# Performance work log

Measured on AMD Instinct MI355X. Metric: run time of the kernel, lower is better.

## Reference

```python
import jax, jax.numpy as jnp
import numpy as np

B, H, W, C_IN, C_HID = 32, 64, 64, 384, 128

def setup_inputs() -> dict:
    key = jax.random.key(0)
    k0, k1, k2 = jax.random.split(key, 3)
    dino_features = jax.random.normal(k0, (B, H, W, C_IN), dtype=jnp.float32)
    # Xavier-uniform(gain=0.5) bounds for conv weights, HWIO layout
    fan1 = C_IN * 9 + C_HID * 9
    lim1 = 0.5 * np.sqrt(6.0 / fan1)
    W1 = jax.random.uniform(k1, (3, 3, C_IN, C_HID), minval=-lim1, maxval=lim1, dtype=jnp.float32)
    b1 = jnp.zeros((C_HID,), dtype=jnp.float32)
    fan2 = C_HID + 1
    lim2 = 0.5 * np.sqrt(6.0 / fan2)
    W2 = jax.random.uniform(k2, (1, 1, C_HID, 1), minval=-lim2, maxval=lim2, dtype=jnp.float32)
    b2 = jnp.zeros((1,), dtype=jnp.float32)
    return {"dino_features": dino_features, "W1": W1, "b1": b1, "W2": W2, "b2": b2}

def _conv(x, w, pad):
    # x: NHWC, w: HWIO -> NHWC
    return jax.lax.conv_general_dilated(
        x, w, window_strides=(1, 1), padding=pad,
        dimension_numbers=("NHWC", "HWIO", "NHWC"))

def reference(dino_features, W1, b1, W2, b2):
    # conv3x3 (pad 1) -> ReLU -> conv1x1 -> sigmoid; output (B,H,W,1)
    h = jax.nn.relu(_conv(dino_features, W1, ((1, 1), (1, 1))) + b1)
    logits = _conv(h, W2, ((0, 0), (0, 0))) + b2
    return jax.nn.sigmoid(logits)
```

## Files before the change

kernel.cpp:

```cpp
#include <hip/hip_runtime.h>
#include <hip/hip_bf16.h>
#include <math.h>


typedef __attribute__((ext_vector_type(8))) unsigned short ushort8;
typedef __attribute__((ext_vector_type(8))) __bf16 bf16x8;
typedef __attribute__((ext_vector_type(4))) float floatx4;

#define HPX 324
#define BUFE 10368

static __device__ __forceinline__ unsigned short f2bf_rne(float f) {
  union { float f; unsigned int u; } x; x.f = f;
  unsigned int u = x.u;
  return (unsigned short)((u + 0x7fffu + ((u >> 16) & 1u)) >> 16);
}

static __device__ __forceinline__ ushort8 pack8(const float* v) {
  ushort8 r;
#pragma unroll
  for (int i = 0; i < 4; ++i) {
    __hip_bfloat162 p = __float22bfloat162_rn(make_float2(v[2 * i], v[2 * i + 1]));
    union { __hip_bfloat162 b; unsigned int u; } c;
    c.b = p;
    r[2 * i] = (unsigned short)(c.u & 0xffffu);
    r[2 * i + 1] = (unsigned short)(c.u >> 16);
  }
  return r;
}

__global__ void prep_w1_kernel(const float* __restrict__ W1,
                               unsigned short* __restrict__ W1b) {
  __shared__ unsigned short tile[32 * 128];
  const int kk = blockIdx.x;
  const int o = kk / 12;
  const int chunk = kk - o * 12;
  const float* src = W1 + (o * 384 + chunk * 32) * 128;
  const int t = threadIdx.x;
#pragma unroll
  for (int i = 0; i < 16; ++i) {
    int idx = t + i * 256;
    int c = idx >> 7;
    int n = idx & 127;
    tile[n * 32 + c] = f2bf_rne(src[idx]);
  }
  __syncthreads();
  unsigned short* dst = W1b + kk * 4096;
#pragma unroll
  for (int i = 0; i < 16; ++i) {
    int idx = t + i * 256;
    dst[idx] = tile[idx];
  }
}

__global__ __launch_bounds__(512, 3) void conv_fused_kernel(
    const float* __restrict__ x, const unsigned short* __restrict__ W1b,
    const float* __restrict__ b1, const float* __restrict__ W2,
    const float* __restrict__ b2, float* __restrict__ out) {
  __shared__ alignas(16) unsigned short Ah[2 * BUFE];
  __shared__ float hsum[256 * 4];

  const int t = threadIdx.x;
  const int w = t >> 6;
  const int wm = w >> 2;
  const int wn = w & 3;
  const int lane = t & 63;
  const int g = lane >> 4;
  const int lr = lane & 15;

  const int img = blockIdx.x >> 4;
  const int tileId = blockIdx.x & 15;
  const int ty0 = (tileId >> 2) << 4;
  const int tx0 = (tileId & 3) << 4;

  int smask = 0;
  int soff[3];
#pragma unroll
  for (int j = 0; j < 3; ++j) {
    int item = t + (j << 9);
    int px = item >> 2, sub = item & 3;
    int hy = (px * 57) >> 10;
    int hx = px - hy * 18;
    int iy = ty0 + hy - 1, ix = tx0 + hx - 1;
    int v = (item < 1296) && ((unsigned)iy < 64u) && ((unsigned)ix < 64u);
    smask |= (v << j);
    int iyc = v ? iy : 0, ixc = v ? ix : 0;
    soff[j] = ((((img << 6) + iyc) << 6) + ixc) * 384 + sub * 8;
  }

  const int boff = ((wn * 32 + lr) << 5) + (g << 3);
  const int aoffl = (lr << 5) + (g << 3);

  floatx4 acc[8][2] = {};

  const float b1v0 = b1[wn * 32 + lr];
  const float b1v1 = b1[wn * 32 + 16 + lr];
  const float w2v0 = W2[wn * 32 + lr];
  const float w2v1 = W2[wn * 32 + 16 + lr];

  float sg1[8];
  float sr[2][8];

  {
    if (smask & 1) {
      *(float4*)&sg1[0] = *(const float4*)(x + soff[0]);
      *(float4*)&sg1[4] = *(const float4*)(x + soff[0] + 4);
    } else {
#pragma unroll
      for (int e = 0; e < 8; ++e) sg1[e] = 0.0f;
    }
#pragma unroll
    for (int j = 0; j < 2; ++j) {
      const int jj = 1 + j;
      if ((smask >> jj) & 1) {
        *(float4*)&sr[j][0] = *(const float4*)(x + soff[jj]);
        *(float4*)&sr[j][4] = *(const float4*)(x + soff[jj] + 4);
      } else {
#pragma unroll
        for (int e = 0; e < 8; ++e) sr[j][e] = 0.0f;
      }
    }
    *(ushort8*)&Ah[t << 3] = pack8(sg1);
    *(ushort8*)&Ah[(t + 512) << 3] = pack8(sr[0]);
    if (t < 272) *(ushort8*)&Ah[(t + 1024) << 3] = pack8(sr[1]);
  }
  __syncthreads();

  for (int c = 0; c < 12; ++c) {
    const int rb = (c & 1) * BUFE;
    const int wb = BUFE - rb;
    const int choff = (c + 1) << 5;
    const bool pf = (c < 11);

#pragma unroll
    for (int ox = 0; ox < 3; ++ox) {
      bf16x8 bf[3][2];
#pragma unroll
      for (int oy = 0; oy < 3; ++oy) {
        const unsigned short* bp =
            W1b + (((oy * 3 + ox) * 12 + c) << 12) + boff;
        bf[oy][0] = *(const bf16x8*)bp;
        bf[oy][1] = *(const bf16x8*)(bp + 512);
      }

      if (ox == 0) {
        if (pf) {
          if (smask & 1) {
            *(float4*)&sg1[0] = *(const float4*)(x + soff[0] + choff);
            *(float4*)&sg1[4] = *(const float4*)(x + soff[0] + choff + 4);
          } else {
#pragma unroll
            for (int e = 0; e < 8; ++e) sg1[e] = 0.0f;
          }
        }
      } else if (ox == 1) {
        if (pf) {
          *(ushort8*)&Ah[wb + (t << 3)] = pack8(sg1);
#pragma unroll
          for (int j = 0; j < 2; ++j) {
            const int jj = 1 + j;
            if ((smask >> jj) & 1) {
              *(float4*)&sr[j][0] = *(const float4*)(x + soff[jj] + choff);
              *(float4*)&sr[j][4] = *(const float4*)(x + soff[jj] + choff + 4);
            } else {
#pragma unroll
              for (int e = 0; e < 8; ++e) sr[j][e] = 0.0f;
            }
          }
        }
      } else {
        if (pf) {
          *(ushort8*)&Ah[wb + ((t + 512) << 3)] = pack8(sr[0]);
          if (t < 272) *(ushort8*)&Ah[wb + ((t + 1024) << 3)] = pack8(sr[1]);
        }
      }

      __builtin_amdgcn_s_setprio(1);
#pragma unroll
      for (int hl = 0; hl < 10; ++hl) {
        const int hg = wm * 8 + hl;
        const bf16x8 af =
            *(const bf16x8*)&Ah[rb + ((hg * 18 + ox) << 5) + aoffl];
#pragma unroll
        for (int oy = 0; oy < 3; ++oy) {
          const int mi = hl - oy;
          if (mi >= 0 && mi < 8) {
            acc[mi][0] = __builtin_amdgcn_mfma_f32_16x16x32_bf16(
                af, bf[oy][0], acc[mi][0], 0, 0, 0);
            acc[mi][1] = __builtin_amdgcn_mfma_f32_16x16x32_bf16(
                af, bf[oy][1], acc[mi][1], 0, 0, 0);
          }
        }
      }
      __builtin_amdgcn_s_setprio(0);
    }
    __syncthreads();
  }

#pragma unroll
  for (int mi = 0; mi < 8; ++mi) {
#pragma unroll
    for (int r = 0; r < 4; ++r) {
      float h0 = fmaxf(acc[mi][0][r] + b1v0, 0.0f);
      float h1 = fmaxf(acc[mi][1][r] + b1v1, 0.0f);
      float v = h0 * w2v0 + h1 * w2v1;
      v += __shfl_xor(v, 1);
      v += __shfl_xor(v, 2);
      v += __shfl_xor(v, 4);
      v += __shfl_xor(v, 8);
      if (lr == 0) {
        int m = (wm * 8 + mi) * 16 + g * 4 + r;
        hsum[m * 4 + wn] = v;
      }
    }
  }
  __syncthreads();
  if (t < 256) {
    float4 p = *(const float4*)&hsum[t * 4];
    float s = p.x + p.y + p.z + p.w + b2[0];
    float sig = 1.0f / (1.0f + expf(-s));
    int prow = t >> 4, pcol = t & 15;
    out[((((img << 6) + ty0 + prow) << 6) + tx0 + pcol)] = sig;
  }
}

extern "C" void kernel_launch(void* const* d_in, const int* in_sizes, int n_in,
                              void* d_out, int out_size, void* d_ws, size_t ws_size,
                              hipStream_t stream) {
  const float* x  = (const float*)d_in[0];
  const float* W1 = (const float*)d_in[1];
  const float* b1 = (const float*)d_in[2];
  const float* W2 = (const float*)d_in[3];
  const float* b2 = (const float*)d_in[4];
  float* out = (float*)d_out;
  unsigned short* W1b = (unsigned short*)d_ws;

  prep_w1_kernel<<<108, 256, 0, stream>>>(W1, W1b);
  conv_fused_kernel<<<512, 512, 0, stream>>>(x, W1b, b1, W2, b2, out);
}
```

Baseline: 342.4 us.

## Halve conv tile to 8x16 pixels and software-pipeline weight register prefetch

Shrinks each block from 16x16 to 8x16 output pixels with 256 threads (4 waves across hidden channels, no row split), doubling grid size to 1024 blocks. The channel loop is unrolled by two with explicit double-buffered register prefetch of the W1 fragments one ox-step ahead, interleaved with the global loads and LDS writes of the next input chunk. The goal is to hide global weight-load latency behind MFMAs and improve occupancy and load balance. The trade-off is a larger halo fraction (10x18 for 8x16 vs 18x18 for 16x16), which means more redundant input loads per output pixel, plus higher register pressure from the two weight buffers.

```diff
diff --git a/kernel.cpp b/kernel.cpp
--- a/kernel.cpp
+++ b/kernel.cpp
@@ -7,8 +7,8 @@
 typedef __attribute__((ext_vector_type(8))) __bf16 bf16x8;
 typedef __attribute__((ext_vector_type(4))) float floatx4;
 
-#define HPX 324
-#define BUFE 10368
+#define HPX2 180
+#define E 5760
 
 static __device__ __forceinline__ unsigned short f2bf_rne(float f) {
   union { float f; unsigned int u; } x; x.f = f;
@@ -53,147 +53,139 @@
   }
 }
 
-__global__ __launch_bounds__(512, 3) void conv_fused_kernel(
+#define SLOAD(DST, JJ, CHOFF)                                                \
+  if ((smask >> (JJ)) & 1) {                                                 \
+    *(float4*)&DST[0] = *(const float4*)(x + soff[JJ] + (CHOFF));            \
+    *(float4*)&DST[4] = *(const float4*)(x + soff[JJ] + (CHOFF) + 4);        \
+  } else {                                                                   \
+    _Pragma("unroll") for (int e = 0; e < 8; ++e) DST[e] = 0.0f;             \
+  }
+
+#define SWRITE(SRC, JJ, WB)                                                  \
+  if ((JJ) < 2 || t < 208)                                                   \
+    *(ushort8*)&Ah[(WB) + ((t + ((JJ) << 8)) << 3)] = pack8(SRC);
+
+#define PREFETCH_B(BUF, OX, CC)                                              \
+  _Pragma("unroll") for (int oy = 0; oy < 3; ++oy) {                         \
+    const unsigned short* bp =                                               \
+        W1b + (((oy * 3 + (OX)) * 12 + (CC)) << 12) + boff;                  \
+    BUF[oy * 2 + 0] = *(const bf16x8*)bp;                                    \
+    BUF[oy * 2 + 1] = *(const bf16x8*)(bp + 512);                            \
+  }
+
+#define MFMA_BLOCK(RB, OX, BUF)                                              \
+  __builtin_amdgcn_s_setprio(1);                                             \
+  _Pragma("unroll") for (int hl = 0; hl < 10; ++hl) {                        \
+    const bf16x8 af =                                                        \
+        *(const bf16x8*)&Ah[(RB) + ((hl * 18 + (OX)) << 5) + aoffl];         \
+    _Pragma("unroll") for (int oy = 0; oy < 3; ++oy) {                       \
+      const int mi = hl - oy;                                                \
+      if (mi >= 0 && mi < 8) {                                               \
+        acc[mi][0] = __builtin_amdgcn_mfma_f32_16x16x32_bf16(                \
+            af, BUF[oy * 2 + 0], acc[mi][0], 0, 0, 0);                       \
+        acc[mi][1] = __builtin_amdgcn_mfma_f32_16x16x32_bf16(                \
+            af, BUF[oy * 2 + 1], acc[mi][1], 0, 0, 0);                       \
+      }                                                                      \
+    }                                                                        \
+  }                                                                          \
+  __builtin_amdgcn_s_setprio(0);
+
+__global__ __launch_bounds__(256, 3) void conv_fused_kernel(
     const float* __restrict__ x, const unsigned short* __restrict__ W1b,
     const float* __restrict__ b1, const float* __restrict__ W2,
     const float* __restrict__ b2, float* __restrict__ out) {
-  __shared__ alignas(16) unsigned short Ah[2 * BUFE];
-  __shared__ float hsum[256 * 4];
+  __shared__ alignas(16) unsigned short Ah[2 * E];
+  __shared__ float hsum[128 * 4];
 
   const int t = threadIdx.x;
   const int w = t >> 6;
-  const int wm = w >> 2;
-  const int wn = w & 3;
   const int lane = t & 63;
   const int g = lane >> 4;
   const int lr = lane & 15;
 
-  const int img = blockIdx.x >> 4;
-  const int tileId = blockIdx.x & 15;
-  const int ty0 = (tileId >> 2) << 4;
-  const int tx0 = (tileId & 3) << 4;
+  const int img = blockIdx.x >> 5;
+  const int tid = blockIdx.x & 31;
+  const int ty0 = (tid >> 2) << 3;
+  const int tx0 = (tid & 3) << 4;
 
   int smask = 0;
   int soff[3];
 #pragma unroll
   for (int j = 0; j < 3; ++j) {
-    int item = t + (j << 9);
+    int item = t + (j << 8);
     int px = item >> 2, sub = item & 3;
     int hy = (px * 57) >> 10;
     int hx = px - hy * 18;
     int iy = ty0 + hy - 1, ix = tx0 + hx - 1;
-    int v = (item < 1296) && ((unsigned)iy < 64u) && ((unsigned)ix < 64u);
+    int v = (item < 720) && ((unsigned)iy < 64u) && ((unsigned)ix < 64u);
     smask |= (v << j);
     int iyc = v ? iy : 0, ixc = v ? ix : 0;
     soff[j] = ((((img << 6) + iyc) << 6) + ixc) * 384 + sub * 8;
   }
 
-  const int boff = ((wn * 32 + lr) << 5) + (g << 3);
+  const int boff = ((w * 32 + lr) << 5) + (g << 3);
   const int aoffl = (lr << 5) + (g << 3);
 
   floatx4 acc[8][2] = {};
 
-  const float b1v0 = b1[wn * 32 + lr];
-  const float b1v1 = b1[wn * 32 + 16 + lr];
-  const float w2v0 = W2[wn * 32 + lr];
-  const float w2v1 = W2[wn * 32 + 16 + lr];
-
-  float sg1[8];
-  float sr[2][8];
+  const float b1v0 = b1[w * 32 + lr];
+  const float b1v1 = b1[w * 32 + 16 + lr];
+  const float w2v0 = W2[w * 32 + lr];
+  const float w2v1 = W2[w * 32 + 16 + lr];
+
+  float sA[8], sB[8];
+  bf16x8 bfU[6], bfV[6];
 
   {
-    if (smask & 1) {
-      *(float4*)&sg1[0] = *(const float4*)(x + soff[0]);
-      *(float4*)&sg1[4] = *(const float4*)(x + soff[0] + 4);
-    } else {
-#pragma unroll
-      for (int e = 0; e < 8; ++e) sg1[e] = 0.0f;
+    SLOAD(sA, 0, 0)
+    SLOAD(sB, 1, 0)
+    SWRITE(sA, 0, 0)
+    SLOAD(sA, 2, 0)
+    SWRITE(sB, 1, 0)
+    SWRITE(sA, 2, 0)
+    PREFETCH_B(bfU, 0, 0)
+  }
+  __syncthreads();
+
+  for (int c = 0; c < 12; c += 2) {
+    const int cB = c + 1;
+    const bool pfB = (c < 10);
+    const int chA = (c + 1) << 5;
+    const int chB = (c + 2) << 5;
+
+    PREFETCH_B(bfV, 1, c)
+    SLOAD(sA, 0, chA)
+    MFMA_BLOCK(0, 0, bfU)
+
+    PREFETCH_B(bfU, 2, c)
+    SLOAD(sB, 1, chA)
+    SWRITE(sA, 0, E)
+    MFMA_BLOCK(0, 1, bfV)
+
+    PREFETCH_B(bfV, 0, cB)
+    SLOAD(sA, 2, chA)
+    SWRITE(sB, 1, E)
+    MFMA_BLOCK(0, 2, bfU)
+
+    SWRITE(sA, 2, E)
+    __syncthreads();
+
+    PREFETCH_B(bfU, 1, cB)
+    if (pfB) { SLOAD(sA, 0, chB) }
+    MFMA_BLOCK(E, 0, bfV)
+
+    PREFETCH_B(bfV, 2, cB)
+    if (pfB) { SLOAD(sB, 1, chB) SWRITE(sA, 0, 0) }
+    MFMA_BLOCK(E, 1, bfU)
+
+    {
+      const int cn = (c + 2 < 12) ? c + 2 : 11;
+      PREFETCH_B(bfU, 0, cn)
     }
-#pragma unroll
-    for (int j = 0; j < 2; ++j) {
-      const int jj = 1 + j;
-      if ((smask >> jj) & 1) {
-        *(float4*)&sr[j][0] = *(const float4*)(x + soff[jj]);
-        *(float4*)&sr[j][4] = *(const float4*)(x + soff[jj] + 4);
-      } else {
-#pragma unroll
-        for (int e = 0; e < 8; ++e) sr[j][e] = 0.0f;
-      }
-    }
-    *(ushort8*)&Ah[t << 3] = pack8(sg1);
-    *(ushort8*)&Ah[(t + 512) << 3] = pack8(sr[0]);
-    if (t < 272) *(ushort8*)&Ah[(t + 1024) << 3] = pack8(sr[1]);
-  }
-  __syncthreads();
-
-  for (int c = 0; c < 12; ++c) {
-    const int rb = (c & 1) * BUFE;
-    const int wb = BUFE - rb;
-    const int choff = (c + 1) << 5;
-    const bool pf = (c < 11);
-
-#pragma unroll
-    for (int ox = 0; ox < 3; ++ox) {
-      bf16x8 bf[3][2];
-#pragma unroll
-      for (int oy = 0; oy < 3; ++oy) {
-        const unsigned short* bp =
-            W1b + (((oy * 3 + ox) * 12 + c) << 12) + boff;
-        bf[oy][0] = *(const bf16x8*)bp;
-        bf[oy][1] = *(const bf16x8*)(bp + 512);
-      }
-
-      if (ox == 0) {
-        if (pf) {
-          if (smask & 1) {
-            *(float4*)&sg1[0] = *(const float4*)(x + soff[0] + choff);
-            *(float4*)&sg1[4] = *(const float4*)(x + soff[0] + choff + 4);
-          } else {
-#pragma unroll
-            for (int e = 0; e < 8; ++e) sg1[e] = 0.0f;
-          }
-        }
-      } else if (ox == 1) {
-        if (pf) {
-          *(ushort8*)&Ah[wb + (t << 3)] = pack8(sg1);
-#pragma unroll
-          for (int j = 0; j < 2; ++j) {
-            const int jj = 1 + j;
-            if ((smask >> jj) & 1) {
-              *(float4*)&sr[j][0] = *(const float4*)(x + soff[jj] + choff);
-              *(float4*)&sr[j][4] = *(const float4*)(x + soff[jj] + choff + 4);
-            } else {
-#pragma unroll
-              for (int e = 0; e < 8; ++e) sr[j][e] = 0.0f;
-            }
-          }
-        }
-      } else {
-        if (pf) {
-          *(ushort8*)&Ah[wb + ((t + 512) << 3)] = pack8(sr[0]);
-          if (t < 272) *(ushort8*)&Ah[wb + ((t + 1024) << 3)] = pack8(sr[1]);
-        }
-      }
-
-      __builtin_amdgcn_s_setprio(1);
-#pragma unroll
-      for (int hl = 0; hl < 10; ++hl) {
-        const int hg = wm * 8 + hl;
-        const bf16x8 af =
-            *(const bf16x8*)&Ah[rb + ((hg * 18 + ox) << 5) + aoffl];
-#pragma unroll
-        for (int oy = 0; oy < 3; ++oy) {
-          const int mi = hl - oy;
-          if (mi >= 0 && mi < 8) {
-            acc[mi][0] = __builtin_amdgcn_mfma_f32_16x16x32_bf16(
-                af, bf[oy][0], acc[mi][0], 0, 0, 0);
-            acc[mi][1] = __builtin_amdgcn_mfma_f32_16x16x32_bf16(
-                af, bf[oy][1], acc[mi][1], 0, 0, 0);
-          }
-        }
-      }
-      __builtin_amdgcn_s_setprio(0);
-    }
+    if (pfB) { SLOAD(sA, 2, chB) SWRITE(sB, 1, 0) }
+    MFMA_BLOCK(E, 2, bfV)
+
+    if (pfB) { SWRITE(sA, 2, 0) }
     __syncthreads();
   }
 
@@ -209,13 +201,13 @@
       v += __shfl_xor(v, 4);
       v += __shfl_xor(v, 8);
       if (lr == 0) {
-        int m = (wm * 8 + mi) * 16 + g * 4 + r;
-        hsum[m * 4 + wn] = v;
+        int m = mi * 16 + g * 4 + r;
+        hsum[m * 4 + w] = v;
       }
     }
   }
   __syncthreads();
-  if (t < 256) {
+  if (t < 128) {
     float4 p = *(const float4*)&hsum[t * 4];
     float s = p.x + p.y + p.z + p.w + b2[0];
     float sig = 1.0f / (1.0f + expf(-s));
@@ -236,5 +228,5 @@
   unsigned short* W1b = (unsigned short*)d_ws;
 
   prep_w1_kernel<<<108, 256, 0, stream>>>(W1, W1b);
-  conv_fused_kernel<<<512, 512, 0, stream>>>(x, W1b, b1, W2, b2, out);
-}
+  conv_fused_kernel<<<1024, 256, 0, stream>>>(x, W1b, b1, W2, b2, out);
+}
```

Measured after the change: 335.2 us. 2.1% less time.

## Pack staged input to bf16 in registers and raise occupancy to 4 blocks

Applied to the files above, without the earlier changes.

Staged input values are now converted to packed bf16 right after the global load, so only 4 registers per slot stay live instead of 8 floats. The three staging slots are spread evenly across the ox iterations, with the last write moved after the MFMA loop. The bias and W2 loads move to the epilogue, and launch bounds rise from 3 to 4 blocks per CU to use the lower register pressure. The risk is register spills or less latency hiding for the global loads, since each load now has a shorter window before it is consumed.

```diff
diff --git a/kernel.cpp b/kernel.cpp
--- a/kernel.cpp
+++ b/kernel.cpp
@@ -53,7 +53,23 @@
   }
 }
 
-__global__ __launch_bounds__(512, 3) void conv_fused_kernel(
+#define SLOADP(DST, JJ, CHOFF)                                               \
+  {                                                                          \
+    float tf[8];                                                             \
+    if ((smask >> (JJ)) & 1) {                                               \
+      *(float4*)&tf[0] = *(const float4*)(x + soff[JJ] + (CHOFF));           \
+      *(float4*)&tf[4] = *(const float4*)(x + soff[JJ] + (CHOFF) + 4);       \
+    } else {                                                                 \
+      _Pragma("unroll") for (int e = 0; e < 8; ++e) tf[e] = 0.0f;            \
+    }                                                                        \
+    DST = pack8(tf);                                                         \
+  }
+
+#define SWRITE8(SRC, JJ, WB)                                                 \
+  if ((JJ) < 2 || t < 272)                                                   \
+    *(ushort8*)&Ah[(WB) + ((t + ((JJ) << 9)) << 3)] = SRC;
+
+__global__ __launch_bounds__(512, 4) void conv_fused_kernel(
     const float* __restrict__ x, const unsigned short* __restrict__ W1b,
     const float* __restrict__ b1, const float* __restrict__ W2,
     const float* __restrict__ b2, float* __restrict__ out) {
@@ -93,36 +109,15 @@
 
   floatx4 acc[8][2] = {};
 
-  const float b1v0 = b1[wn * 32 + lr];
-  const float b1v1 = b1[wn * 32 + 16 + lr];
-  const float w2v0 = W2[wn * 32 + lr];
-  const float w2v1 = W2[wn * 32 + 16 + lr];
-
-  float sg1[8];
-  float sr[2][8];
+  ushort8 su0, su1, su2;
 
   {
-    if (smask & 1) {
-      *(float4*)&sg1[0] = *(const float4*)(x + soff[0]);
-      *(float4*)&sg1[4] = *(const float4*)(x + soff[0] + 4);
-    } else {
-#pragma unroll
-      for (int e = 0; e < 8; ++e) sg1[e] = 0.0f;
-    }
-#pragma unroll
-    for (int j = 0; j < 2; ++j) {
-      const int jj = 1 + j;
-      if ((smask >> jj) & 1) {
-        *(float4*)&sr[j][0] = *(const float4*)(x + soff[jj]);
-        *(float4*)&sr[j][4] = *(const float4*)(x + soff[jj] + 4);
-      } else {
-#pragma unroll
-        for (int e = 0; e < 8; ++e) sr[j][e] = 0.0f;
-      }
-    }
-    *(ushort8*)&Ah[t << 3] = pack8(sg1);
-    *(ushort8*)&Ah[(t + 512) << 3] = pack8(sr[0]);
-    if (t < 272) *(ushort8*)&Ah[(t + 1024) << 3] = pack8(sr[1]);
+    SLOADP(su0, 0, 0)
+    SLOADP(su1, 1, 0)
+    SLOADP(su2, 2, 0)
+    SWRITE8(su0, 0, 0)
+    SWRITE8(su1, 1, 0)
+    SWRITE8(su2, 2, 0)
   }
   __syncthreads();
 
@@ -143,35 +138,15 @@
         bf[oy][1] = *(const bf16x8*)(bp + 512);
       }
 
-      if (ox == 0) {
-        if (pf) {
-          if (smask & 1) {
-            *(float4*)&sg1[0] = *(const float4*)(x + soff[0] + choff);
-            *(float4*)&sg1[4] = *(const float4*)(x + soff[0] + choff + 4);
-          } else {
-#pragma unroll
-            for (int e = 0; e < 8; ++e) sg1[e] = 0.0f;
-          }
-        }
-      } else if (ox == 1) {
-        if (pf) {
-          *(ushort8*)&Ah[wb + (t << 3)] = pack8(sg1);
-#pragma unroll
-          for (int j = 0; j < 2; ++j) {
-            const int jj = 1 + j;
-            if ((smask >> jj) & 1) {
-              *(float4*)&sr[j][0] = *(const float4*)(x + soff[jj] + choff);
-              *(float4*)&sr[j][4] = *(const float4*)(x + soff[jj] + choff + 4);
-            } else {
-#pragma unroll
-              for (int e = 0; e < 8; ++e) sr[j][e] = 0.0f;
-            }
-          }
-        }
-      } else {
-        if (pf) {
-          *(ushort8*)&Ah[wb + ((t + 512) << 3)] = pack8(sr[0]);
-          if (t < 272) *(ushort8*)&Ah[wb + ((t + 1024) << 3)] = pack8(sr[1]);
+      if (pf) {
+        if (ox == 0) {
+          SLOADP(su0, 0, choff)
+        } else if (ox == 1) {
+          SWRITE8(su0, 0, wb)
+          SLOADP(su1, 1, choff)
+        } else {
+          SWRITE8(su1, 1, wb)
+          SLOADP(su2, 2, choff)
         }
       }
 
@@ -194,9 +169,14 @@
       }
       __builtin_amdgcn_s_setprio(0);
     }
+    if (pf) { SWRITE8(su2, 2, wb) }
     __syncthreads();
   }
 
+  const float b1v0 = b1[wn * 32 + lr];
+  const float b1v1 = b1[wn * 32 + 16 + lr];
+  const float w2v0 = W2[wn * 32 + lr];
+  const float w2v1 = W2[wn * 32 + 16 + lr];
 #pragma unroll
   for (int mi = 0; mi < 8; ++mi) {
 #pragma unroll
```

Result: faster. 333.2 us (-2.7%).
